# Kernel optimization log

Hardware: AMD Instinct MI355X
Metric: run time of the kernel (lower is better)

The kernel has to match this reference:

```python
import jax, jax.numpy as jnp
import numpy as np

B, S, D, H = 2, 2048, 2048, 16
HD = D // H


def setup_inputs() -> dict:
    key = jax.random.key(0)
    ks = jax.random.split(key, 9)
    scale = 0.02
    return {
        "x": jax.random.normal(ks[0], (B, S, D), dtype=jnp.float32),
        "wq_w": jax.random.normal(ks[1], (D, D), dtype=jnp.float32) * scale,
        "wq_b": jnp.zeros((D,), dtype=jnp.float32),
        "wk_w": jax.random.normal(ks[2], (D, D), dtype=jnp.float32) * scale,
        "wk_b": jnp.zeros((D,), dtype=jnp.float32),
        "wv_w": jax.random.normal(ks[3], (D, D), dtype=jnp.float32) * scale,
        "wv_b": jnp.zeros((D,), dtype=jnp.float32),
        "wo_w": jax.random.normal(ks[4], (D, D), dtype=jnp.float32) * scale,
        "wo_b": jnp.zeros((D,), dtype=jnp.float32),
    }


def reference(x, wq_w, wq_b, wk_w, wk_b, wv_w, wv_b, wo_w, wo_b):
    # torch Linear: y = x @ W.T + b
    q = x @ wq_w.T + wq_b  # [B,S,D]
    k = x @ wk_w.T + wk_b
    v = x @ wv_w.T + wv_b
    # [B,S,D] -> [B,H,S,HD]
    q = q.reshape(B, S, H, HD).transpose(0, 2, 1, 3)
    k = k.reshape(B, S, H, HD).transpose(0, 2, 1, 3)
    v = v.reshape(B, S, H, HD).transpose(0, 2, 1, 3)
    # scores [B,H,S,S], scaled by sqrt(d_dim) as in the original (not head_dim)
    scores = jnp.einsum("bhid,bhjd->bhij", q, k) / np.float32(np.sqrt(D))
    # faithful reproduction of the module's triu/transpose masking:
    m = jnp.swapaxes(jnp.triu(scores), -2, -1)  # lower-tri, zeros elsewhere
    p = jax.nn.softmax(m, axis=-2)              # softmax over dim=-2, zeros included
    a = jnp.swapaxes(jnp.triu(p), -2, -1)       # [B,H,S,S]
    attn = jnp.einsum("bhij,bhjd->bhid", a, v)  # [B,H,S,HD]
    concat = attn.transpose(0, 2, 1, 3).reshape(B, S, D)
    return concat @ wo_w.T + wo_b
```

## Files before the change

### kernel.cpp

```cpp
#include <hip/hip_runtime.h>

#define BB 2
#define SS 2048
#define DD 2048
#define HH 16
#define HDIM 128
#define MTOK (BB*SS)
#define BHH (BB*HH)
#define NCHUNK 16
#define QKN (2*DD)

typedef __attribute__((ext_vector_type(8))) __bf16 bf16x8;
typedef __attribute__((ext_vector_type(4))) float f32x4;
typedef __attribute__((ext_vector_type(8))) int i32x8;

__device__ __forceinline__ unsigned short f2bf(float f) {
  unsigned u = __float_as_uint(f);
  u += 0x7FFFu + ((u >> 16) & 1u);
  return (unsigned short)(u >> 16);
}
__device__ __forceinline__ float bf2f(unsigned short s) {
  return __uint_as_float(((unsigned)s) << 16);
}
__device__ __forceinline__ unsigned char f2e4m3(float f) {
  int pk = __builtin_amdgcn_cvt_pk_fp8_f32(f, f, 0, false);
  return (unsigned char)(pk & 0xFF);
}

#define GLOAD_LDS16(src, dst)                                                   \
  __builtin_amdgcn_global_load_lds(                                             \
      (const void __attribute__((address_space(1)))*)(src),                     \
      (void __attribute__((address_space(3)))*)(dst), 16, 0, 0)

__global__ void cvt_x_dual(const float* __restrict__ in,
                           unsigned short* __restrict__ outb,
                           unsigned int* __restrict__ out8, int n4) {
  int i = blockIdx.x * blockDim.x + threadIdx.x;
  if (i < n4) {
    float4 v = ((const float4*)in)[i];
    ushort4 o;
    o.x = f2bf(v.x); o.y = f2bf(v.y); o.z = f2bf(v.z); o.w = f2bf(v.w);
    ((ushort4*)outb)[i] = o;
    int p0 = __builtin_amdgcn_cvt_pk_fp8_f32(v.x, v.y, 0, false);
    int p1 = __builtin_amdgcn_cvt_pk_fp8_f32(v.z, v.w, 0, false);
    out8[i] = (unsigned)(p0 & 0xFFFF) | ((unsigned)(p1 & 0xFFFF) << 16);
  }
}

__global__ void cvt_wqk8(const float* __restrict__ a, const float* __restrict__ b,
                         unsigned int* __restrict__ out) {
  int i = blockIdx.x * blockDim.x + threadIdx.x;
  int sel = i >> 20, r = i & 0xFFFFF;
  const float* src = sel == 0 ? a : b;
  float4 v = ((const float4*)src)[r];
  int p0 = __builtin_amdgcn_cvt_pk_fp8_f32(v.x, v.y, 0, false);
  int p1 = __builtin_amdgcn_cvt_pk_fp8_f32(v.z, v.w, 0, false);
  out[i] = (unsigned)(p0 & 0xFFFF) | ((unsigned)(p1 & 0xFFFF) << 16);
}

__global__ void cvt_w2bf(const float* __restrict__ a, const float* __restrict__ b,
                         unsigned short* __restrict__ out) {
  int i = blockIdx.x * blockDim.x + threadIdx.x;
  int sel = i >> 20, r = i & 0xFFFFF;
  const float* src = sel == 0 ? a : b;
  float4 v = ((const float4*)src)[r];
  ushort4 o;
  o.x = f2bf(v.x); o.y = f2bf(v.y); o.z = f2bf(v.z); o.w = f2bf(v.w);
  ((ushort4*)out)[i] = o;
}

__global__ void concat2(const float* __restrict__ a, const float* __restrict__ b,
                        float* __restrict__ out) {
  int i = blockIdx.x * blockDim.x + threadIdx.x;
  if (i < DD) { out[i] = a[i]; out[DD + i] = b[i]; }
}

template <bool OUT_BF16>
__global__ __launch_bounds__(256, 2) void gemm_bt(
    const __bf16* __restrict__ A, const __bf16* __restrict__ W,
    const float* __restrict__ bias, void* __restrict__ Cout,
    int M, int N, int K) {
  __shared__ __bf16 lA[128 * 32];
  __shared__ __bf16 lB[128 * 32];
  const int t = threadIdx.x;
  const int lane = t & 63, wave = t >> 6;
  const int quad = lane >> 4, l16 = lane & 15;
  const int m0 = blockIdx.y * 128, n0 = blockIdx.x * 128;
  const int wm = (wave & 1) * 64, wn = (wave >> 1) * 64;

  f32x4 acc[4][4] = {};

  for (int k0 = 0; k0 < K; k0 += 32) {
#pragma unroll
    for (int c = 0; c < 2; ++c) {
      int lin = c * 256 + t;
      int row = lin >> 2;
      int col = (lin & 3) * 8;
      const __bf16* srcA = A + (size_t)(m0 + row) * K + k0 + col;
      const __bf16* srcB = W + (size_t)(n0 + row) * K + k0 + col;
      GLOAD_LDS16(srcA, &lA[(c * 256 + wave * 64) * 8]);
      GLOAD_LDS16(srcB, &lB[(c * 256 + wave * 64) * 8]);
    }
    __syncthreads();
    bf16x8 af[4], bfr[4];
#pragma unroll
    for (int mt = 0; mt < 4; ++mt)
      af[mt] = *(const bf16x8*)&lA[(wm + mt * 16 + l16) * 32 + quad * 8];
#pragma unroll
    for (int nt = 0; nt < 4; ++nt)
      bfr[nt] = *(const bf16x8*)&lB[(wn + nt * 16 + l16) * 32 + quad * 8];
#pragma unroll
    for (int mt = 0; mt < 4; ++mt)
#pragma unroll
      for (int nt = 0; nt < 4; ++nt)
        acc[mt][nt] = __builtin_amdgcn_mfma_f32_16x16x32_bf16(af[mt], bfr[nt],
                                                              acc[mt][nt], 0, 0, 0);
    __syncthreads();
  }

#pragma unroll
  for (int mt = 0; mt < 4; ++mt) {
#pragma unroll
    for (int nt = 0; nt < 4; ++nt) {
      int col = n0 + wn + nt * 16 + l16;
      float bv = bias[col];
#pragma unroll
      for (int r = 0; r < 4; ++r) {
        int row = m0 + wm + mt * 16 + quad * 4 + r;
        float v = acc[mt][nt][r] + bv;
        if constexpr (OUT_BF16)
          ((unsigned short*)Cout)[(size_t)row * N + col] = f2bf(v);
        else
          ((float*)Cout)[(size_t)row * N + col] = v;
      }
    }
  }
}

__global__ __launch_bounds__(256, 2) void gemm_qk_fp8(
    const unsigned char* __restrict__ A8, const unsigned char* __restrict__ W8,
    const float* __restrict__ bias, unsigned char* __restrict__ Cout,
    int M, int N, int K) {
  __shared__ unsigned char lA[128 * 128];
  __shared__ unsigned char lB[128 * 128];
  const int t = threadIdx.x;
  const int lane = t & 63, wave = t >> 6;
  const int quad = lane >> 4, l16 = lane & 15;
  const int m0 = blockIdx.y * 128, n0 = blockIdx.x * 128;
  const int wm = (wave & 1) * 64, wn = (wave >> 1) * 64;

  f32x4 acc[4][4] = {};

  for (int k0 = 0; k0 < K; k0 += 128) {
#pragma unroll
    for (int c = 0; c < 4; ++c) {
      int lin = c * 256 + t;
      int row = lin >> 3;
      int ch = lin & 7;
      const unsigned char* srcA = A8 + (size_t)(m0 + row) * K + k0 + ch * 16;
      const unsigned char* srcB = W8 + (size_t)(n0 + row) * K + k0 + ch * 16;
      GLOAD_LDS16(srcA, &lA[(c * 256 + wave * 64) * 16]);
      GLOAD_LDS16(srcB, &lB[(c * 256 + wave * 64) * 16]);
    }
    __syncthreads();
    i32x8 af[4];
#pragma unroll
    for (int mt = 0; mt < 4; ++mt)
      af[mt] = *(const i32x8*)&lA[(wm + mt * 16 + l16) * 128 + quad * 32];
#pragma unroll
    for (int nt = 0; nt < 4; ++nt) {
      i32x8 bfr = *(const i32x8*)&lB[(wn + nt * 16 + l16) * 128 + quad * 32];
#pragma unroll
      for (int mt = 0; mt < 4; ++mt)
        acc[mt][nt] = __builtin_amdgcn_mfma_scale_f32_16x16x128_f8f6f4(
            af[mt], bfr, acc[mt][nt], 0, 0, 0, 127, 0, 127);
    }
    __syncthreads();
  }

#pragma unroll
  for (int mt = 0; mt < 4; ++mt) {
#pragma unroll
    for (int nt = 0; nt < 4; ++nt) {
      int col = n0 + wn + nt * 16 + l16;
      float bv = bias[col];
#pragma unroll
      for (int r = 0; r < 4; ++r) {
        int row = m0 + wm + mt * 16 + quad * 4 + r;
        Cout[(size_t)row * N + col] = f2e4m3(acc[mt][nt][r] + bv);
      }
    }
  }
}

__global__ __launch_bounds__(256, 4) void qk_rowsum_mx(
    const unsigned char* __restrict__ q8, const unsigned char* __restrict__ k8,
    float* __restrict__ denomA, float* __restrict__ denomB,
    float* __restrict__ diag) {
  __shared__ unsigned char lK[128 * 128];
  __shared__ float lred[2 * 256];
  const int t = threadIdx.x;
  const int lane = t & 63, wave = t >> 6;
  const int quad = lane >> 4, l16 = lane & 15;
  const int bh = blockIdx.y;
  const int b = bh >> 4, h = bh & 15;
  const int p = blockIdx.x & 15, hf = blockIdx.x >> 4;
  const float SL2E = 0.03188233603f;

  const int nseg = hf ? 2 : 1;
  for (int si = 0; si < nseg; ++si) {
    int q, jt0, cnt, mode;
    bool dg;
    if (hf == 0)      { q = p;      jt0 = p >> 1;       cnt = 9;             dg = true;  mode = 1; }
    else if (si == 0) { q = p;      jt0 = (p >> 1) + 9; cnt = 7 - (p >> 1);  dg = false; mode = 2; }
    else              { q = 31 - p; jt0 = q >> 1;       cnt = 16 - (q >> 1); dg = true;  mode = 5; }

    i32x8 af[4];
#pragma unroll
    for (int mt = 0; mt < 4; ++mt)
      af[mt] = *(const i32x8*)(q8 + (size_t)(b * SS + q * 64 + mt * 16 + l16) * QKN
                               + h * HDIM + quad * 32);

    float rs[4][4] = {};
    float dv[4][4] = {};

    for (int jt = jt0; jt < jt0 + cnt; ++jt) {
      const int j0 = jt * 128;
#pragma unroll
      for (int c = 0; c < 4; ++c) {
        int L = c * 256 + t;
        int row = L >> 3, ch = L & 7;
        const unsigned char* src = k8 + (size_t)(b * SS + j0 + row) * QKN
                                   + h * HDIM + ((ch ^ (row & 7)) * 16);
        GLOAD_LDS16(src, &lK[(c * 256 + wave * 64) * 16]);
      }
      __syncthreads();
      const bool masked = dg && (jt == jt0);
#pragma unroll
      for (int ntl = 0; ntl < 2; ++ntl) {
        int jrow = (wave * 2 + ntl) * 16 + l16;
        uint4 lo = *(const uint4*)&lK[jrow * 128 + (((quad * 2) ^ (jrow & 7)) * 16)];
        uint4 hi = *(const uint4*)&lK[jrow * 128 + (((quad * 2 + 1) ^ (jrow & 7)) * 16)];
        i32x8 bfr;
        bfr[0] = lo.x; bfr[1] = lo.y; bfr[2] = lo.z; bfr[3] = lo.w;
        bfr[4] = hi.x; bfr[5] = hi.y; bfr[6] = hi.z; bfr[7] = hi.w;
        f32x4 sacc[4];
#pragma unroll
        for (int mt = 0; mt < 4; ++mt) {
          f32x4 z = {0.f, 0.f, 0.f, 0.f};
          sacc[mt] = __builtin_amdgcn_mfma_scale_f32_16x16x128_f8f6f4(
              af[mt], bfr, z, 0, 0, 0, 127, 0, 127);
        }
        int colg = j0 + jrow;
        if (masked) {
#pragma unroll
          for (int mt = 0; mt < 4; ++mt)
#pragma unroll
            for (int r = 0; r < 4; ++r) {
              int rg = q * 64 + mt * 16 + quad * 4 + r;
              float e = exp2f(sacc[mt][r] * SL2E);
              if (colg >= rg) rs[mt][r] += e;
              if (colg == rg) dv[mt][r] = e;
            }
        } else {
#pragma unroll
          for (int mt = 0; mt < 4; ++mt)
#pragma unroll
            for (int r = 0; r < 4; ++r)
              rs[mt][r] += exp2f(sacc[mt][r] * SL2E);
        }
      }
      __syncthreads();
    }

#pragma unroll
    for (int mt = 0; mt < 4; ++mt)
#pragma unroll
      for (int r = 0; r < 4; ++r) {
        float s = rs[mt][r], d = dv[mt][r];
#pragma unroll
        for (int off = 1; off < 16; off <<= 1) {
          s += __shfl_xor(s, off, 64);
          d += __shfl_xor(d, off, 64);
        }
        if (l16 == 0) {
          int rl = mt * 16 + quad * 4 + r;
          lred[wave * 64 + rl] = s;
          lred[256 + wave * 64 + rl] = d;
        }
      }
    __syncthreads();
    if (t < 64) {
      float tot = lred[t] + lred[64 + t] + lred[128 + t] + lred[192 + t];
      float dtot = lred[256 + t] + lred[320 + t] + lred[384 + t] + lred[448 + t];
      int rg = q * 64 + t;
      if (mode & 1) {
        denomA[bh * SS + rg] = (float)rg + tot;
        diag[bh * SS + rg] = dtot;
      }
      if (mode & 2) denomB[bh * SS + rg] = tot;
      if (mode & 4) denomB[bh * SS + rg] = 0.f;
    }
    __syncthreads();
  }
}

__global__ void scan_pass1(const __bf16* __restrict__ v0,
                           float* __restrict__ csum) {
  int blk = blockIdx.x;
  int bh = blk >> 4, c = blk & 15;
  int b = bh >> 4, h = bh & 15;
  int t = threadIdx.x;
  int rs = t >> 4, dg = t & 15;
  const unsigned short* base = (const unsigned short*)v0 +
      (size_t)(b * SS + c * 128 + rs * 8) * DD + h * HDIM + dg * 8;
  float s[8] = {0.f, 0.f, 0.f, 0.f, 0.f, 0.f, 0.f, 0.f};
#pragma unroll
  for (int i = 0; i < 8; ++i) {
    uint4 u = *(const uint4*)(base + (size_t)i * DD);
    const unsigned short* us = (const unsigned short*)&u;
#pragma unroll
    for (int j = 0; j < 8; ++j) s[j] += bf2f(us[j]);
  }
  __shared__ float red[16 * 128];
#pragma unroll
  for (int j = 0; j < 8; ++j) red[rs * 128 + dg * 8 + j] = s[j];
  __syncthreads();
  for (int st = 8; st >= 1; st >>= 1) {
    if (rs < st) {
#pragma unroll
      for (int j = 0; j < 8; ++j)
        red[rs * 128 + dg * 8 + j] += red[(rs + st) * 128 + dg * 8 + j];
    }
    __syncthreads();
  }
  if (rs == 0) {
#pragma unroll
    for (int j = 0; j < 8; ++j)
      csum[(size_t)blk * 128 + dg * 8 + j] = red[dg * 8 + j];
  }
}

__global__ void scan_pass2(const __bf16* __restrict__ v0,
                           const float* __restrict__ csum,
                           const float* __restrict__ denomA,
                           const float* __restrict__ denomB,
                           const float* __restrict__ diag,
                           unsigned short* __restrict__ ctx) {
  int blk = blockIdx.x;
  int bh = blk >> 4, c = blk & 15;
  int b = bh >> 4, h = bh & 15;
  int t = threadIdx.x;
  int rs = t >> 4, dg = t & 15;
  const unsigned short* vbase = (const unsigned short*)v0 +
      (size_t)(b * SS + c * 128 + rs * 8) * DD + h * HDIM + dg * 8;
  float vrow[8][8];
  float ls[8] = {0.f, 0.f, 0.f, 0.f, 0.f, 0.f, 0.f, 0.f};
#pragma unroll
  for (int i = 0; i < 8; ++i) {
    uint4 u = *(const uint4*)(vbase + (size_t)i * DD);
    const unsigned short* us = (const unsigned short*)&u;
#pragma unroll
    for (int j = 0; j < 8; ++j) {
      vrow[i][j] = bf2f(us[j]);
      ls[j] += vrow[i][j];
    }
  }
  __shared__ float red[16 * 128];
#pragma unroll
  for (int j = 0; j < 8; ++j) red[rs * 128 + dg * 8 + j] = ls[j];
  __syncthreads();

  float pre[8] = {0.f, 0.f, 0.f, 0.f, 0.f, 0.f, 0.f, 0.f};
  for (int cc = 0; cc < c; ++cc) {
    const float* cp = csum + (size_t)(bh * 16 + cc) * 128 + dg * 8;
#pragma unroll
    for (int j = 0; j < 8; ++j) pre[j] += cp[j];
  }
  for (int ss2 = 0; ss2 < rs; ++ss2) {
#pragma unroll
    for (int j = 0; j < 8; ++j) pre[j] += red[ss2 * 128 + dg * 8 + j];
  }

  int row0 = c * 128 + rs * 8;
  unsigned short* obase =
      ctx + (size_t)(b * SS + row0) * DD + h * HDIM + dg * 8;
  const float* dnA = denomA + bh * SS + row0;
  const float* dnB = denomB + bh * SS + row0;
  const float* dgp = diag + bh * SS + row0;
#pragma unroll
  for (int i = 0; i < 8; ++i) {
    float inv = 1.0f / (dnA[i] + dnB[i]);
    float dvv = dgp[i];
    unsigned short o[8];
#pragma unroll
    for (int j = 0; j < 8; ++j) {
      float val = (pre[j] + dvv * vrow[i][j]) * inv;
      o[j] = f2bf(val);
      pre[j] += vrow[i][j];
    }
    *(uint4*)(obase + (size_t)i * DD) = *(const uint4*)o;
  }
}

extern "C" void kernel_launch(void* const* d_in, const int* in_sizes, int n_in,
                              void* d_out, int out_size, void* d_ws, size_t ws_size,
                              hipStream_t stream) {
  (void)in_sizes; (void)n_in; (void)out_size; (void)ws_size;
  const float* x    = (const float*)d_in[0];
  const float* wq_w = (const float*)d_in[1];
  const float* wq_b = (const float*)d_in[2];
  const float* wk_w = (const float*)d_in[3];
  const float* wk_b = (const float*)d_in[4];
  const float* wv_w = (const float*)d_in[5];
  const float* wv_b = (const float*)d_in[6];
  const float* wo_w = (const float*)d_in[7];
  const float* wo_b = (const float*)d_in[8];

  char* ws = (char*)d_ws;
  size_t off = 0;
  auto alloc = [&](size_t bytes) {
    char* p = ws + off;
    off += (bytes + 255) & ~(size_t)255;
    return p;
  };
  unsigned short* xb   = (unsigned short*)alloc((size_t)MTOK * DD * 2);
  unsigned char*  x8   = (unsigned char*)alloc((size_t)MTOK * DD);
  unsigned char*  wqk8 = (unsigned char*)alloc((size_t)2 * DD * DD);
  unsigned short* wvo  = (unsigned short*)alloc((size_t)2 * DD * DD * 2);
  unsigned char*  qk8  = (unsigned char*)alloc((size_t)MTOK * QKN);
  unsigned short* v    = (unsigned short*)alloc((size_t)MTOK * DD * 2);
  unsigned short* ctx  = (unsigned short*)alloc((size_t)MTOK * DD * 2);
  float* biasqk = (float*)alloc((size_t)2 * DD * 4);
  float* denomA = (float*)alloc((size_t)BHH * SS * 4);
  float* denomB = (float*)alloc((size_t)BHH * SS * 4);
  float* diag   = (float*)alloc((size_t)BHH * SS * 4);
  float* csum   = (float*)alloc((size_t)BHH * NCHUNK * 128 * 4);

  {
    int n4 = MTOK * DD / 4;
    cvt_x_dual<<<n4 / 256, 256, 0, stream>>>(x, xb, (unsigned int*)x8, n4);
    cvt_wqk8<<<(2 << 20) / 256, 256, 0, stream>>>(wq_w, wk_w, (unsigned int*)wqk8);
    cvt_w2bf<<<(2 << 20) / 256, 256, 0, stream>>>(wv_w, wo_w, wvo);
    concat2<<<(DD + 255) / 256, 256, 0, stream>>>(wq_b, wk_b, biasqk);
  }

  gemm_qk_fp8<<<dim3(QKN / 128, MTOK / 128), 256, 0, stream>>>(
      x8, wqk8, biasqk, qk8, MTOK, QKN, DD);

  gemm_bt<true><<<dim3(DD / 128, MTOK / 128), 256, 0, stream>>>(
      (const __bf16*)xb, (const __bf16*)wvo, wv_b, v, MTOK, DD, DD);

  qk_rowsum_mx<<<dim3(32, BHH), 256, 0, stream>>>(
      qk8,
      qk8 + DD,
      denomA, denomB, diag);

  scan_pass1<<<BHH * NCHUNK, 256, 0, stream>>>((const __bf16*)v, csum);
  scan_pass2<<<BHH * NCHUNK, 256, 0, stream>>>((const __bf16*)v, csum,
                                               denomA, denomB, diag, ctx);

  gemm_bt<false><<<dim3(DD / 128, MTOK / 128), 256, 0, stream>>>(
      (const __bf16*)ctx, (const __bf16*)(wvo + (size_t)DD * DD), wo_b,
      d_out, MTOK, DD, DD);
}
```

Baseline: 367.9 us.

## Split row-sum work into balanced segments with atomic denominator accumulation

The QK row-sum kernel is repartitioned from 1024 blocks with uneven 9/16-tile work into 2048 blocks. Each paired query tile's 17 key tiles are split into four nearly equal segments, and block ids are interleaved across heads. Partial sums go into a single denominator buffer with atomicAdd, pre-initialised by a new init kernel with the row-index term. This removes the two-buffer merge and is meant to improve load balance and occupancy, at the cost of atomics, an extra launch and more Q fragment loads.

```diff
diff --git a/kernel.cpp b/kernel.cpp
--- a/kernel.cpp
+++ b/kernel.cpp
@@ -75,6 +75,11 @@
   if (i < DD) { out[i] = a[i]; out[DD + i] = b[i]; }
 }
 
+__global__ void init_denom(float* __restrict__ denom) {
+  int i = blockIdx.x * blockDim.x + threadIdx.x;
+  denom[i] = (float)(i & (SS - 1));
+}
+
 template <bool OUT_BF16>
 __global__ __launch_bounds__(256, 2) void gemm_bt(
     const __bf16* __restrict__ A, const __bf16* __restrict__ W,
@@ -195,36 +200,43 @@
 
 __global__ __launch_bounds__(256, 4) void qk_rowsum_mx(
     const unsigned char* __restrict__ q8, const unsigned char* __restrict__ k8,
-    float* __restrict__ denomA, float* __restrict__ denomB,
-    float* __restrict__ diag) {
+    float* __restrict__ denom, float* __restrict__ diag) {
   __shared__ unsigned char lK[128 * 128];
-  __shared__ float lred[2 * 256];
+  __shared__ float lred[256];
   const int t = threadIdx.x;
   const int lane = t & 63, wave = t >> 6;
   const int quad = lane >> 4, l16 = lane & 15;
-  const int bh = blockIdx.y;
+  const int id = blockIdx.x;
+  const int r8 = id & 7, m = id >> 3;
+  const int bh = r8 + 8 * (m >> 6);
+  const int seg = m & 63;
+  const int p = seg >> 2, s = seg & 3;
   const int b = bh >> 4, h = bh & 15;
-  const int p = blockIdx.x & 15, hf = blockIdx.x >> 4;
   const float SL2E = 0.03188233603f;
 
-  const int nseg = hf ? 2 : 1;
-  for (int si = 0; si < nseg; ++si) {
-    int q, jt0, cnt, mode;
-    bool dg;
-    if (hf == 0)      { q = p;      jt0 = p >> 1;       cnt = 9;             dg = true;  mode = 1; }
-    else if (si == 0) { q = p;      jt0 = (p >> 1) + 9; cnt = 7 - (p >> 1);  dg = false; mode = 2; }
-    else              { q = 31 - p; jt0 = q >> 1;       cnt = 16 - (q >> 1); dg = true;  mode = 5; }
+  const int t0 = 16 - (p >> 1);
+  const int start = (s * 17) >> 2, end = ((s + 1) * 17) >> 2;
+
+  for (int run = 0; run < 2; ++run) {
+    int q, i_lo, i_hi;
+    bool dgf;
+    if (run == 0) {
+      q = p; i_lo = start; i_hi = (end < t0) ? end : t0; dgf = (start == 0);
+    } else {
+      q = 31 - p; i_lo = (start > t0) ? start : t0; i_hi = end; dgf = (start <= t0);
+    }
+    if (i_lo >= i_hi) continue;
+    const int jt_lo = (q >> 1) + (run == 0 ? i_lo : i_lo - t0);
+    const int jt_hi = jt_lo + (i_hi - i_lo);
 
     i32x8 af[4];
 #pragma unroll
     for (int mt = 0; mt < 4; ++mt)
       af[mt] = *(const i32x8*)(q8 + (size_t)(b * SS + q * 64 + mt * 16 + l16) * QKN
                                + h * HDIM + quad * 32);
-
     float rs[4][4] = {};
-    float dv[4][4] = {};
-
-    for (int jt = jt0; jt < jt0 + cnt; ++jt) {
+
+    for (int jt = jt_lo; jt < jt_hi; ++jt) {
       const int j0 = jt * 128;
 #pragma unroll
       for (int c = 0; c < 4; ++c) {
@@ -235,72 +247,84 @@
         GLOAD_LDS16(src, &lK[(c * 256 + wave * 64) * 16]);
       }
       __syncthreads();
-      const bool masked = dg && (jt == jt0);
-#pragma unroll
-      for (int ntl = 0; ntl < 2; ++ntl) {
-        int jrow = (wave * 2 + ntl) * 16 + l16;
-        uint4 lo = *(const uint4*)&lK[jrow * 128 + (((quad * 2) ^ (jrow & 7)) * 16)];
-        uint4 hi = *(const uint4*)&lK[jrow * 128 + (((quad * 2 + 1) ^ (jrow & 7)) * 16)];
-        i32x8 bfr;
-        bfr[0] = lo.x; bfr[1] = lo.y; bfr[2] = lo.z; bfr[3] = lo.w;
-        bfr[4] = hi.x; bfr[5] = hi.y; bfr[6] = hi.z; bfr[7] = hi.w;
-        f32x4 sacc[4];
-#pragma unroll
-        for (int mt = 0; mt < 4; ++mt) {
-          f32x4 z = {0.f, 0.f, 0.f, 0.f};
-          sacc[mt] = __builtin_amdgcn_mfma_scale_f32_16x16x128_f8f6f4(
-              af[mt], bfr, z, 0, 0, 0, 127, 0, 127);
-        }
-        int colg = j0 + jrow;
-        if (masked) {
-#pragma unroll
-          for (int mt = 0; mt < 4; ++mt)
+      const bool masked = dgf && (jt == jt_lo);
+
+      if (masked) {
+        float dv[4][4] = {};
+#pragma unroll
+        for (int ntl = 0; ntl < 2; ++ntl) {
+          int jrow = (wave * 2 + ntl) * 16 + l16;
+          uint4 lo = *(const uint4*)&lK[jrow * 128 + (((quad * 2) ^ (jrow & 7)) * 16)];
+          uint4 hi = *(const uint4*)&lK[jrow * 128 + (((quad * 2 + 1) ^ (jrow & 7)) * 16)];
+          i32x8 bfr;
+          bfr[0] = lo.x; bfr[1] = lo.y; bfr[2] = lo.z; bfr[3] = lo.w;
+          bfr[4] = hi.x; bfr[5] = hi.y; bfr[6] = hi.z; bfr[7] = hi.w;
+          int colg = j0 + jrow;
+#pragma unroll
+          for (int mt = 0; mt < 4; ++mt) {
+            f32x4 z = {0.f, 0.f, 0.f, 0.f};
+            f32x4 sacc = __builtin_amdgcn_mfma_scale_f32_16x16x128_f8f6f4(
+                af[mt], bfr, z, 0, 0, 0, 127, 0, 127);
 #pragma unroll
             for (int r = 0; r < 4; ++r) {
               int rg = q * 64 + mt * 16 + quad * 4 + r;
-              float e = exp2f(sacc[mt][r] * SL2E);
+              float e = exp2f(sacc[r] * SL2E);
               if (colg >= rg) rs[mt][r] += e;
               if (colg == rg) dv[mt][r] = e;
             }
-        } else {
-#pragma unroll
-          for (int mt = 0; mt < 4; ++mt)
+          }
+        }
+        __syncthreads();
+#pragma unroll
+        for (int mt = 0; mt < 4; ++mt)
+#pragma unroll
+          for (int r = 0; r < 4; ++r) {
+            float d = dv[mt][r];
+#pragma unroll
+            for (int off = 1; off < 16; off <<= 1) d += __shfl_xor(d, off, 64);
+            if (l16 == 0) lred[wave * 64 + mt * 16 + quad * 4 + r] = d;
+          }
+        __syncthreads();
+        if (t < 64)
+          diag[bh * SS + q * 64 + t] =
+              lred[t] + lred[64 + t] + lred[128 + t] + lred[192 + t];
+        __syncthreads();
+      } else {
+#pragma unroll
+        for (int ntl = 0; ntl < 2; ++ntl) {
+          int jrow = (wave * 2 + ntl) * 16 + l16;
+          uint4 lo = *(const uint4*)&lK[jrow * 128 + (((quad * 2) ^ (jrow & 7)) * 16)];
+          uint4 hi = *(const uint4*)&lK[jrow * 128 + (((quad * 2 + 1) ^ (jrow & 7)) * 16)];
+          i32x8 bfr;
+          bfr[0] = lo.x; bfr[1] = lo.y; bfr[2] = lo.z; bfr[3] = lo.w;
+          bfr[4] = hi.x; bfr[5] = hi.y; bfr[6] = hi.z; bfr[7] = hi.w;
+#pragma unroll
+          for (int mt = 0; mt < 4; ++mt) {
+            f32x4 z = {0.f, 0.f, 0.f, 0.f};
+            f32x4 sacc = __builtin_amdgcn_mfma_scale_f32_16x16x128_f8f6f4(
+                af[mt], bfr, z, 0, 0, 0, 127, 0, 127);
 #pragma unroll
             for (int r = 0; r < 4; ++r)
-              rs[mt][r] += exp2f(sacc[mt][r] * SL2E);
+              rs[mt][r] += exp2f(sacc[r] * SL2E);
+          }
         }
+        __syncthreads();
       }
-      __syncthreads();
     }
 
 #pragma unroll
     for (int mt = 0; mt < 4; ++mt)
 #pragma unroll
       for (int r = 0; r < 4; ++r) {
-        float s = rs[mt][r], d = dv[mt][r];
-#pragma unroll
-        for (int off = 1; off < 16; off <<= 1) {
-          s += __shfl_xor(s, off, 64);
-          d += __shfl_xor(d, off, 64);
-        }
-        if (l16 == 0) {
-          int rl = mt * 16 + quad * 4 + r;
-          lred[wave * 64 + rl] = s;
-          lred[256 + wave * 64 + rl] = d;
-        }
+        float sv = rs[mt][r];
+#pragma unroll
+        for (int off = 1; off < 16; off <<= 1) sv += __shfl_xor(sv, off, 64);
+        if (l16 == 0) lred[wave * 64 + mt * 16 + quad * 4 + r] = sv;
       }
     __syncthreads();
-    if (t < 64) {
-      float tot = lred[t] + lred[64 + t] + lred[128 + t] + lred[192 + t];
-      float dtot = lred[256 + t] + lred[320 + t] + lred[384 + t] + lred[448 + t];
-      int rg = q * 64 + t;
-      if (mode & 1) {
-        denomA[bh * SS + rg] = (float)rg + tot;
-        diag[bh * SS + rg] = dtot;
-      }
-      if (mode & 2) denomB[bh * SS + rg] = tot;
-      if (mode & 4) denomB[bh * SS + rg] = 0.f;
-    }
+    if (t < 64)
+      atomicAdd(&denom[bh * SS + q * 64 + t],
+                lred[t] + lred[64 + t] + lred[128 + t] + lred[192 + t]);
     __syncthreads();
   }
 }
@@ -343,8 +367,7 @@
 
 __global__ void scan_pass2(const __bf16* __restrict__ v0,
                            const float* __restrict__ csum,
-                           const float* __restrict__ denomA,
-                           const float* __restrict__ denomB,
+                           const float* __restrict__ denom,
                            const float* __restrict__ diag,
                            unsigned short* __restrict__ ctx) {
   int blk = blockIdx.x;
@@ -385,12 +408,11 @@
   int row0 = c * 128 + rs * 8;
   unsigned short* obase =
       ctx + (size_t)(b * SS + row0) * DD + h * HDIM + dg * 8;
-  const float* dnA = denomA + bh * SS + row0;
-  const float* dnB = denomB + bh * SS + row0;
+  const float* dn = denom + bh * SS + row0;
   const float* dgp = diag + bh * SS + row0;
 #pragma unroll
   for (int i = 0; i < 8; ++i) {
-    float inv = 1.0f / (dnA[i] + dnB[i]);
+    float inv = 1.0f / dn[i];
     float dvv = dgp[i];
     unsigned short o[8];
 #pragma unroll
@@ -432,8 +454,7 @@
   unsigned short* v    = (unsigned short*)alloc((size_t)MTOK * DD * 2);
   unsigned short* ctx  = (unsigned short*)alloc((size_t)MTOK * DD * 2);
   float* biasqk = (float*)alloc((size_t)2 * DD * 4);
-  float* denomA = (float*)alloc((size_t)BHH * SS * 4);
-  float* denomB = (float*)alloc((size_t)BHH * SS * 4);
+  float* denom  = (float*)alloc((size_t)BHH * SS * 4);
   float* diag   = (float*)alloc((size_t)BHH * SS * 4);
   float* csum   = (float*)alloc((size_t)BHH * NCHUNK * 128 * 4);
 
@@ -443,6 +464,7 @@
     cvt_wqk8<<<(2 << 20) / 256, 256, 0, stream>>>(wq_w, wk_w, (unsigned int*)wqk8);
     cvt_w2bf<<<(2 << 20) / 256, 256, 0, stream>>>(wv_w, wo_w, wvo);
     concat2<<<(DD + 255) / 256, 256, 0, stream>>>(wq_b, wk_b, biasqk);
+    init_denom<<<(BHH * SS) / 256, 256, 0, stream>>>(denom);
   }
 
   gemm_qk_fp8<<<dim3(QKN / 128, MTOK / 128), 256, 0, stream>>>(
@@ -451,14 +473,14 @@
   gemm_bt<true><<<dim3(DD / 128, MTOK / 128), 256, 0, stream>>>(
       (const __bf16*)xb, (const __bf16*)wvo, wv_b, v, MTOK, DD, DD);
 
-  qk_rowsum_mx<<<dim3(32, BHH), 256, 0, stream>>>(
+  qk_rowsum_mx<<<2048, 256, 0, stream>>>(
       qk8,
       qk8 + DD,
-      denomA, denomB, diag);
+      denom, diag);
 
   scan_pass1<<<BHH * NCHUNK, 256, 0, stream>>>((const __bf16*)v, csum);
   scan_pass2<<<BHH * NCHUNK, 256, 0, stream>>>((const __bf16*)v, csum,
-                                               denomA, denomB, diag, ctx);
+                                               denom, diag, ctx);
 
   gemm_bt<false><<<dim3(DD / 128, MTOK / 128), 256, 0, stream>>>(
       (const __bf16*)ctx, (const __bf16*)(wvo + (size_t)DD * DD), wo_b,
```

After: 380.4 us. +3.4%, slower.
